# Performance work log

Measured on AMD Instinct MI355X. Metric: run time of the kernel, lower is better.

Reference implementation:

```python
import jax, jax.numpy as jnp
import numpy as np

N = 4096
IN_SIZE = 512
MLP_W = 16
HID = 512
MID = 64  # hardcoded tgc2 output size in the torch module
OUT = 128
BN_EPS = 1e-5


def setup_inputs() -> dict:
    key = jax.random.key(0)
    ks = jax.random.split(key, 24)
    adj = (jax.random.uniform(ks[0], (N, N)) < 0.05).astype(jnp.float32)
    xdeg = jax.random.uniform(ks[1], (N, N), dtype=jnp.float32)
    ydeg = jax.random.uniform(ks[2], (N, N), dtype=jnp.float32)
    u = lambda k, sh, fan: jax.random.uniform(k, sh, jnp.float32, -1.0, 1.0) / np.sqrt(fan)
    return {
        "adj": adj, "xdeg": xdeg, "ydeg": ydeg,
        # edge MLP: 3 -> MLP_W -> 2
        "mlp_w1": u(ks[3], (3, MLP_W), 3), "mlp_b1": jnp.zeros((MLP_W,), jnp.float32),
        "mlp_w2": u(ks[4], (MLP_W, 2), MLP_W), "mlp_b2": jnp.zeros((2,), jnp.float32),
        # positional linear: Linear(N, in_size) applied to eye(N) -> pe = W^T + b
        "pe_w": u(ks[5], (N, IN_SIZE), N), "pe_b": jnp.zeros((IN_SIZE,), jnp.float32),
        # GCN weights
        "gc1_w": u(ks[6], (IN_SIZE, HID), HID),
        "lin2_w": u(ks[7], (HID, MID), HID), "lin2_b": jnp.zeros((MID,), jnp.float32),
        "gc3_w": u(ks[8], (MID, OUT), OUT),
        # BatchNorm (eval mode: running stats)
        "bn1_g": jnp.ones((HID,), jnp.float32), "bn1_b": jnp.zeros((HID,), jnp.float32),
        "bn1_m": jnp.zeros((HID,), jnp.float32), "bn1_v": jnp.ones((HID,), jnp.float32),
        "bn2_g": jnp.ones((OUT,), jnp.float32), "bn2_b": jnp.zeros((OUT,), jnp.float32),
        "bn2_m": jnp.zeros((OUT,), jnp.float32), "bn2_v": jnp.ones((OUT,), jnp.float32),
    }


def reference(adj, xdeg, ydeg, mlp_w1, mlp_b1, mlp_w2, mlp_b2, pe_w, pe_b,
              gc1_w, lin2_w, lin2_b, gc3_w,
              bn1_g, bn1_b, bn1_m, bn1_v, bn2_g, bn2_b, bn2_m, bn2_v):
    # Edge MLP + softmax over [adj, xdeg, ydeg] features; torch only computes it
    # at nonzero adj entries then scatters into a dense mask. Since the mask is
    # multiplied by adj, computing densely and multiplying is exactly equivalent.
    feats = jnp.stack([adj, xdeg, ydeg], axis=-1)          # [N, N, 3]
    h = jax.nn.relu(jnp.einsum('nmf,fw->nmw', feats, mlp_w1) + mlp_b1)
    logits = jnp.einsum('nmw,wc->nmc', h, mlp_w2) + mlp_b2  # [N, N, 2]
    mask = jax.nn.softmax(logits, axis=-1)[..., 1]          # [N, N]
    a = adj * mask + jnp.eye(adj.shape[0], dtype=adj.dtype)

    # Degree normalization: A' = D_row^{-1/2} A D_col^{-1/2} (broadcast, no diag matmuls)
    rowsum = jnp.sum(a, axis=1)
    colsum = jnp.sum(a, axis=0)
    d_row = jnp.where(rowsum > 0, rowsum ** -0.5, 0.0)
    d_col = jnp.where(colsum > 0, colsum ** -0.5, 0.0)
    a = d_row[:, None] * a * d_col[None, :]

    # pe = Linear(eye(N)) = W^T + b (eval mode, dropout off)
    pe = pe_w + pe_b[None, :]                               # [N, IN_SIZE]

    h = a @ (pe @ gc1_w)                                    # GCN layer 1
    h = (h - bn1_m) * (bn1_g / jnp.sqrt(bn1_v + BN_EPS)) + bn1_b
    h = h @ lin2_w + lin2_b                                 # tgc2
    mid = h
    h = jax.nn.relu(h)
    h = a @ (h @ gc3_w)                                     # GCN layer 3
    out = (h - bn2_m) * (bn2_g / jnp.sqrt(bn2_v + BN_EPS)) + bn2_b
    return out, mid
```

## Files before the change

kernel.cpp:

```cpp
#include <hip/hip_runtime.h>
#include <hip/hip_bf16.h>

#define NN 4096
#define INS 512
#define HIDW 512
#define MIDW 64
#define OUTW 128
#define CAP 384
#define SEG 96
#define BN_EPS 1e-5f
#define CS_BLOCKS 256
#define CS_ROWS (NN / CS_BLOCKS)
#define NSTRIP 8
#define NPAIR (NSTRIP / 2)
#define SLOTCAP (NSTRIP * SEG)

__global__ __launch_bounds__(256) void k_count(
    const float* __restrict__ adj,
    int* __restrict__ cslot, int* __restrict__ cnt, int* __restrict__ dflag)
{
    const int t = threadIdx.x;
    const int wave = t >> 6, lane = t & 63;
    const int gw = blockIdx.x * 4 + wave;
    const int i = gw >> 3, s = gw & 7;
    const int colbase = s * 512;
    const float* __restrict__ base = adj + (size_t)i * NN + colbase + 4 * lane;
    float4 a4a = *reinterpret_cast<const float4*>(base);
    float4 a4b = *reinterpret_cast<const float4*>(base + 256);
    const float av[8] = {a4a.x, a4a.y, a4a.z, a4a.w,
                         a4b.x, a4b.y, a4b.z, a4b.w};
    int* __restrict__ slot = cslot + (size_t)i * SLOTCAP + s * SEG;
    const unsigned long long lt = (1ULL << lane) - 1ULL;
    int run = 0;
    #pragma unroll
    for (int c = 0; c < 8; ++c) {
        int col = colbase + ((c < 4) ? (4 * lane + c) : (256 + 4 * lane + c - 4));
        bool diag = (col == i);
        bool act = (av[c] != 0.f) || diag;
        if (diag) dflag[i] = (av[c] != 0.f) ? 1 : 0;
        unsigned long long m = __ballot(act);
        if (act) {
            int pos = run + __popcll(m & lt);
            if (pos < SEG) slot[pos] = col;
        }
        run += __popcll(m);
    }
    if (lane == 0) cnt[gw] = (run < SEG) ? run : SEG;
}

__global__ __launch_bounds__(256) void k_fill(
    const float* __restrict__ xdeg, const float* __restrict__ ydeg,
    const int* __restrict__ cslot, const int* __restrict__ cnt,
    const int* __restrict__ dflag,
    const float* __restrict__ w1, const float* __restrict__ b1,
    const float* __restrict__ w2, const float* __restrict__ b2,
    float* __restrict__ a_vals, int* __restrict__ a_cols,
    float* __restrict__ rs_part)
{
    __shared__ float shb[16], sw1x[16], sw1y[16], sw2[32], sb2[2];
    const int t = threadIdx.x;
    const int wave = t >> 6, lane = t & 63;
    if (t < 16) {
        shb[t]  = b1[t] + w1[t];
        sw1x[t] = w1[16 + t];
        sw1y[t] = w1[32 + t];
    }
    if (t < 32) sw2[t] = w2[t];
    if (t < 2)  sb2[t] = b2[t];
    __syncthreads();

    const int q = __builtin_amdgcn_readfirstlane(blockIdx.x * 4 + wave);
    const int i = q >> 2;
    const int sp = (q & 3) * 2;
    const int* __restrict__ cb = cnt + i * NSTRIP;
    int wb = 0;
    #pragma unroll
    for (int ss = 0; ss < NSTRIP; ++ss) if (ss < sp) wb += cb[ss];
    const int n0 = cb[sp];
    const int n1 = cb[sp + 1];
    const int ntot = n0 + n1;
    const int hasde = dflag[i];
    const int* __restrict__ slot = cslot + (size_t)i * SLOTCAP + sp * SEG;
    const float* __restrict__ xrow = xdeg + (size_t)i * NN;
    const float* __restrict__ yrow = ydeg + (size_t)i * NN;
    float* __restrict__ gv = a_vals + (size_t)i * CAP;
    int*   __restrict__ gc = a_cols + (size_t)i * CAP;

    float local = 0.f;
    for (int p = lane; p < ntot; p += 64) {
        int col = (p < n0) ? slot[p] : slot[SEG + p - n0];
        float x = xrow[col];
        float y = yrow[col];
        float l0 = sb2[0], l1 = sb2[1];
        #pragma unroll
        for (int w = 0; w < 16; ++w) {
            float hw = fmaf(x, sw1x[w], shb[w]);
            hw = fmaf(y, sw1y[w], hw);
            hw = fmaxf(hw, 0.f);
            l0 = fmaf(hw, sw2[2 * w],     l0);
            l1 = fmaf(hw, sw2[2 * w + 1], l1);
        }
        float v = 1.f / (1.f + __expf(l0 - l1));
        if (col == i) v = hasde ? (v + 1.f) : 1.f;
        int gp = wb + p;
        if (gp < CAP) { gc[gp] = col; gv[gp] = v; }
        local += v;
    }
    #pragma unroll
    for (int o = 32; o >= 1; o >>= 1)
        local += __shfl_down(local, o, 64);
    if (lane == 0) rs_part[q] = local;
}

__global__ __launch_bounds__(256) void k_colsum(
    const float* __restrict__ a_vals, const int* __restrict__ a_cols,
    const int* __restrict__ cnt, float* __restrict__ P)
{
    __shared__ float ls[NN];
    const int t = threadIdx.x;
    const int b = blockIdx.x;
    for (int j = t; j < NN; j += 256) ls[j] = 0.f;
    __syncthreads();
    const int r0 = b * CS_ROWS;
    for (int r = r0; r < r0 + CS_ROWS; ++r) {
        int n = 0;
        #pragma unroll
        for (int ss = 0; ss < NSTRIP; ++ss) n += cnt[r * NSTRIP + ss];
        n = (n < CAP) ? n : CAP;
        const float* __restrict__ vr = a_vals + (size_t)r * CAP;
        const int*   __restrict__ cr = a_cols + (size_t)r * CAP;
        for (int p = t; p < n; p += 256)
            atomicAdd(&ls[cr[p]], vr[p]);
    }
    __syncthreads();
    for (int j = t; j < NN; j += 256)
        P[(size_t)b * NN + j] = ls[j];
}

__global__ __launch_bounds__(512) void k_misc(
    const float* __restrict__ lin2_w, const float* __restrict__ lin2_b,
    const float* __restrict__ bn1_g, const float* __restrict__ bn1_b,
    const float* __restrict__ bn1_m, const float* __restrict__ bn1_v,
    const float* __restrict__ bn2_g, const float* __restrict__ bn2_b,
    const float* __restrict__ bn2_m, const float* __restrict__ bn2_v,
    const float* __restrict__ rs_part, const float* __restrict__ P,
    float* __restrict__ Wp, float* __restrict__ c1,
    float* __restrict__ s2g, float* __restrict__ t2g,
    float* __restrict__ d_row, float* __restrict__ d_col)
{
    const int t = threadIdx.x;
    if (blockIdx.x == 0) {
        __shared__ float t1s[HIDW];
        {
            int h = t;
            float s1 = bn1_g[h] * rsqrtf(bn1_v[h] + BN_EPS);
            t1s[h] = bn1_b[h] - bn1_m[h] * s1;
            for (int m = 0; m < MIDW; ++m)
                Wp[(size_t)h * MIDW + m] = s1 * lin2_w[(size_t)h * MIDW + m];
        }
        __syncthreads();
        if (t < MIDW) {
            float acc = lin2_b[t];
            for (int h = 0; h < HIDW; ++h)
                acc = fmaf(t1s[h], lin2_w[(size_t)h * MIDW + t], acc);
            c1[t] = acc;
        } else if (t >= 64 && t < 64 + OUTW) {
            int j = t - 64;
            float s2 = bn2_g[j] * rsqrtf(bn2_v[j] + BN_EPS);
            s2g[j] = s2;
            t2g[j] = bn2_b[j] - bn2_m[j] * s2;
        }
    } else {
        int j = (blockIdx.x - 1) * 512 + t;
        float r = 0.f;
        #pragma unroll
        for (int s = 0; s < NPAIR; ++s) r += rs_part[j * NPAIR + s];
        d_row[j] = (r > 0.f) ? 1.f / sqrtf(r) : 0.f;
        float c = 0.f;
        for (int b = 0; b < CS_BLOCKS; ++b)
            c += P[(size_t)b * NN + j];
        d_col[j] = (c > 0.f) ? 1.f / sqrtf(c) : 0.f;
    }
}

template <bool ABIAS, bool ROWSCALE>
__global__ __launch_bounds__(256) void k_thin(
    const float* __restrict__ A, const float* __restrict__ B,
    const float* __restrict__ abias, const float* __restrict__ rscale,
    float* __restrict__ C, int M, int K)
{
    __shared__ float As[64][36];
    __shared__ float Bs[64][64];
    const int t = threadIdx.x;
    const int bm = blockIdx.x * 32;
    const int c2 = t & 31, rg = t >> 5;

    float acc[4][2] = {};

    for (int k0 = 0; k0 < K; k0 += 64) {
        #pragma unroll
        for (int l = 0; l < 8; ++l) {
            int e = t + l * 256;
            int r = e >> 6, k = e & 63;
            float v = A[(size_t)(bm + r) * K + k0 + k];
            if (ABIAS) v += abias[k0 + k];
            As[k][r] = v;
        }
        #pragma unroll
        for (int l = 0; l < 16; ++l) {
            int e = t + l * 256;
            int k = e >> 6, n = e & 63;
            Bs[k][n] = B[(size_t)(k0 + k) * 64 + n];
        }
        __syncthreads();
        #pragma unroll
        for (int k = 0; k < 64; ++k) {
            float4 a4 = *reinterpret_cast<const float4*>(&As[k][rg * 4]);
            float2 b2 = *reinterpret_cast<const float2*>(&Bs[k][2 * c2]);
            acc[0][0] = fmaf(a4.x, b2.x, acc[0][0]);
            acc[0][1] = fmaf(a4.x, b2.y, acc[0][1]);
            acc[1][0] = fmaf(a4.y, b2.x, acc[1][0]);
            acc[1][1] = fmaf(a4.y, b2.y, acc[1][1]);
            acc[2][0] = fmaf(a4.z, b2.x, acc[2][0]);
            acc[2][1] = fmaf(a4.z, b2.y, acc[2][1]);
            acc[3][0] = fmaf(a4.w, b2.x, acc[3][0]);
            acc[3][1] = fmaf(a4.w, b2.y, acc[3][1]);
        }
        __syncthreads();
    }

    #pragma unroll
    for (int u = 0; u < 4; ++u) {
        int r = bm + rg * 4 + u;
        float sc = ROWSCALE ? rscale[r] : 1.f;
        float2 o = make_float2(acc[u][0] * sc, acc[u][1] * sc);
        *reinterpret_cast<float2*>(&C[(size_t)r * 64 + 2 * c2]) = o;
    }
}

template <bool WITH_MID>
__global__ __launch_bounds__(256) void k_spmm(
    const float* __restrict__ a_vals, const int* __restrict__ a_cols,
    const int* __restrict__ cnt, const float* __restrict__ X,
    const float* __restrict__ d_row, const float* __restrict__ d_col,
    const float* __restrict__ c1,
    const float* __restrict__ gc3, const float* __restrict__ s2g,
    const float* __restrict__ t2g,
    float* __restrict__ O1, float* __restrict__ O2)
{
    __shared__ float sv[2][CAP];
    __shared__ int   scl[2][CAP];
    __shared__ float sacc[4][64];
    const int t = threadIdx.x;
    const int wave = t >> 6, lane = t & 63;
    const int rb = wave >> 1, h = wave & 1;
    const int i = blockIdx.x * 2 + rb;
    int n = 0;
    #pragma unroll
    for (int ss = 0; ss < NSTRIP; ++ss) n += cnt[i * NSTRIP + ss];
    n = (n < CAP) ? n : CAP;
    const int n16 = (n + 15) & ~15;
    const float* __restrict__ vrow = a_vals + (size_t)i * CAP;
    const int*   __restrict__ crow = a_cols + (size_t)i * CAP;

    for (int p = h * 64 + lane; p < n16; p += 128) {
        bool ok = p < n;
        sv[rb][p]  = ok ? vrow[p] : 0.f;
        scl[rb][p] = ok ? crow[p] : 0;
    }
    __syncthreads();

    const int eh = lane >> 5;
    const int lc = lane & 31;
    const int Q  = n16 >> 1;
    const int Qh = Q >> 1;

    float a0 = 0.f, a1 = 0.f;
    for (int q = h * Qh; q < (h + 1) * Qh; q += 4) {
        #pragma unroll
        for (int j = 0; j < 4; ++j) {
            int p = 2 * (q + j) + eh;
            float v = sv[rb][p];
            int c = scl[rb][p];
            float2 x = *reinterpret_cast<const float2*>(X + (size_t)c * 64 + 2 * lc);
            a0 = fmaf(v, x.x, a0);
            a1 = fmaf(v, x.y, a1);
        }
    }
    a0 += __shfl_xor(a0, 32);
    a1 += __shfl_xor(a1, 32);
    if (lane < 32) { sacc[wave][2 * lc] = a0; sacc[wave][2 * lc + 1] = a1; }
    __syncthreads();

    if (WITH_MID) {
        if (h == 0 && lane < 32) {
            float s0 = sacc[wave][2 * lc]     + sacc[wave + 1][2 * lc];
            float s1 = sacc[wave][2 * lc + 1] + sacc[wave + 1][2 * lc + 1];
            float dr = d_row[i];
            float dc = d_col[i];
            float m0 = fmaf(s0, dr, c1[2 * lc]);
            float m1 = fmaf(s1, dr, c1[2 * lc + 1]);
            *reinterpret_cast<float2*>(O1 + (size_t)i * 64 + 2 * lc) =
                make_float2(m0, m1);
            *reinterpret_cast<float2*>(O2 + (size_t)i * 64 + 2 * lc) =
                make_float2(dc * fmaxf(m0, 0.f), dc * fmaxf(m1, 0.f));
        }
    } else {
        if (h == 0 && lane < 32) {
            float dr = d_row[i];
            float s0 = (sacc[wave][2 * lc]     + sacc[wave + 1][2 * lc])     * dr;
            float s1 = (sacc[wave][2 * lc + 1] + sacc[wave + 1][2 * lc + 1]) * dr;
            sacc[wave][2 * lc]     = s0;
            sacc[wave][2 * lc + 1] = s1;
        }
        __syncthreads();
        const int rb2 = t >> 7;
        const int j = t & 127;
        const float* __restrict__ srow = sacc[2 * rb2];
        float acc = 0.f;
        #pragma unroll 8
        for (int k = 0; k < 64; ++k)
            acc = fmaf(srow[k], gc3[k * 128 + j], acc);
        int orow = blockIdx.x * 2 + rb2;
        O1[(size_t)orow * 128 + j] = fmaf(acc, s2g[j], t2g[j]);
    }
}

extern "C" void kernel_launch(void* const* d_in, const int* in_sizes, int n_in,
                              void* d_out, int out_size, void* d_ws, size_t ws_size,
                              hipStream_t stream) {
    const float* adj    = (const float*)d_in[0];
    const float* xdeg   = (const float*)d_in[1];
    const float* ydeg   = (const float*)d_in[2];
    const float* mlp_w1 = (const float*)d_in[3];
    const float* mlp_b1 = (const float*)d_in[4];
    const float* mlp_w2 = (const float*)d_in[5];
    const float* mlp_b2 = (const float*)d_in[6];
    const float* pe_w   = (const float*)d_in[7];
    const float* pe_b   = (const float*)d_in[8];
    const float* gc1_w  = (const float*)d_in[9];
    const float* lin2_w = (const float*)d_in[10];
    const float* lin2_b = (const float*)d_in[11];
    const float* gc3_w  = (const float*)d_in[12];
    const float* bn1_g  = (const float*)d_in[13];
    const float* bn1_b  = (const float*)d_in[14];
    const float* bn1_m  = (const float*)d_in[15];
    const float* bn1_v  = (const float*)d_in[16];
    const float* bn2_g  = (const float*)d_in[17];
    const float* bn2_b  = (const float*)d_in[18];
    const float* bn2_m  = (const float*)d_in[19];
    const float* bn2_v  = (const float*)d_in[20];

    float* out = (float*)d_out;
    float* mid = out + (size_t)NN * OUTW;

    char* w = (char*)d_ws;
    float* a_vals = (float*)w;  w += (size_t)NN * CAP * 4;
    int*   a_cols = (int*)w;    w += (size_t)NN * CAP * 4;
    int*   cslot  = (int*)w;    w += (size_t)NN * SLOTCAP * 4;
    int*   cnt    = (int*)w;    w += (size_t)NN * NSTRIP * 4;
    int*   dflag  = (int*)w;    w += (size_t)NN * 4;
    float* rs_part= (float*)w;  w += (size_t)NN * NPAIR * 4;
    float* d_row  = (float*)w;  w += (size_t)NN * 4;
    float* d_col  = (float*)w;  w += (size_t)NN * 4;
    float* P      = (float*)w;  w += (size_t)CS_BLOCKS * NN * 4;
    float* Wp     = (float*)w;  w += (size_t)HIDW * MIDW * 4;
    float* W2     = (float*)w;  w += (size_t)INS * MIDW * 4;
    float* c1     = (float*)w;  w += 256;
    float* s2g    = (float*)w;  w += 512;
    float* t2g    = (float*)w;  w += 512;
    float* G      = (float*)w;  w += (size_t)NN * MIDW * 4;
    float* R      = (float*)w;  w += (size_t)NN * MIDW * 4;

    k_count<<<NN * NSTRIP / 4, 256, 0, stream>>>(adj, cslot, cnt, dflag);
    k_fill<<<NN * NPAIR / 4, 256, 0, stream>>>(
        xdeg, ydeg, cslot, cnt, dflag, mlp_w1, mlp_b1, mlp_w2, mlp_b2,
        a_vals, a_cols, rs_part);
    k_colsum<<<CS_BLOCKS, 256, 0, stream>>>(a_vals, a_cols, cnt, P);
    k_misc<<<9, 512, 0, stream>>>(lin2_w, lin2_b, bn1_g, bn1_b, bn1_m, bn1_v,
                                  bn2_g, bn2_b, bn2_m, bn2_v, rs_part, P,
                                  Wp, c1, s2g, t2g, d_row, d_col);
    k_thin<false, false><<<INS / 32, 256, 0, stream>>>(
        gc1_w, Wp, nullptr, nullptr, W2, INS, HIDW);
    k_thin<true, true><<<NN / 32, 256, 0, stream>>>(
        pe_w, W2, pe_b, d_col, G, NN, INS);
    k_spmm<true><<<NN / 2, 256, 0, stream>>>(
        a_vals, a_cols, cnt, G, d_row, d_col, c1,
        nullptr, nullptr, nullptr, mid, R);
    k_spmm<false><<<NN / 2, 256, 0, stream>>>(
        a_vals, a_cols, cnt, R, d_row, d_col, nullptr,
        gc3_w, s2g, t2g, out, nullptr);
}
```

Baseline: 133.1 us.

## Merge independent dense GEMMs into sparse-prep kernels to cut launches

The kernel sequence is regrouped so independent work shares a launch. The BN/lin2 weight prep runs as an extra block of the count kernel, the gc1_w×Wp product runs as extra blocks of the fill kernel, and the pe×W2 product runs alongside the column-sum kernel. To allow this, the d_col row scaling moves out of the G GEMM and into the first SpMM's value staging, so G no longer waits on d_col. This removes two kernel launches and their serial dependencies. The cost is one extra d_col gather per nonzero in the SpMM, and heterogeneous blocks inside one grid that may balance unevenly.

```diff
diff --git a/kernel.cpp b/kernel.cpp
--- a/kernel.cpp
+++ b/kernel.cpp
@@ -15,144 +15,71 @@
 #define NPAIR (NSTRIP / 2)
 #define SLOTCAP (NSTRIP * SEG)
 
-__global__ __launch_bounds__(256) void k_count(
+__device__ __forceinline__ void thin_block(
+    const float* __restrict__ A, const float* __restrict__ B,
+    const float* __restrict__ abias, float* __restrict__ C, int K, int bb)
+{
+    __shared__ float As[64][36];
+    __shared__ float Bs[64][64];
+    const int t = threadIdx.x;
+    const int bm = bb * 32;
+    const int c2 = t & 31, rg = t >> 5;
+
+    float acc[4][2] = {};
+    for (int k0 = 0; k0 < K; k0 += 64) {
+        #pragma unroll
+        for (int l = 0; l < 8; ++l) {
+            int e = t + l * 256;
+            int r = e >> 6, k = e & 63;
+            float v = A[(size_t)(bm + r) * K + k0 + k];
+            if (abias) v += abias[k0 + k];
+            As[k][r] = v;
+        }
+        #pragma unroll
+        for (int l = 0; l < 16; ++l) {
+            int e = t + l * 256;
+            int k = e >> 6, n = e & 63;
+            Bs[k][n] = B[(size_t)(k0 + k) * 64 + n];
+        }
+        __syncthreads();
+        #pragma unroll
+        for (int k = 0; k < 64; ++k) {
+            float4 a4 = *reinterpret_cast<const float4*>(&As[k][rg * 4]);
+            float2 b2 = *reinterpret_cast<const float2*>(&Bs[k][2 * c2]);
+            acc[0][0] = fmaf(a4.x, b2.x, acc[0][0]);
+            acc[0][1] = fmaf(a4.x, b2.y, acc[0][1]);
+            acc[1][0] = fmaf(a4.y, b2.x, acc[1][0]);
+            acc[1][1] = fmaf(a4.y, b2.y, acc[1][1]);
+            acc[2][0] = fmaf(a4.z, b2.x, acc[2][0]);
+            acc[2][1] = fmaf(a4.z, b2.y, acc[2][1]);
+            acc[3][0] = fmaf(a4.w, b2.x, acc[3][0]);
+            acc[3][1] = fmaf(a4.w, b2.y, acc[3][1]);
+        }
+        __syncthreads();
+    }
+    #pragma unroll
+    for (int u = 0; u < 4; ++u) {
+        int r = bm + rg * 4 + u;
+        *reinterpret_cast<float2*>(&C[(size_t)r * 64 + 2 * c2]) =
+            make_float2(acc[u][0], acc[u][1]);
+    }
+}
+
+__global__ __launch_bounds__(256) void k_count_prep(
     const float* __restrict__ adj,
-    int* __restrict__ cslot, int* __restrict__ cnt, int* __restrict__ dflag)
-{
-    const int t = threadIdx.x;
-    const int wave = t >> 6, lane = t & 63;
-    const int gw = blockIdx.x * 4 + wave;
-    const int i = gw >> 3, s = gw & 7;
-    const int colbase = s * 512;
-    const float* __restrict__ base = adj + (size_t)i * NN + colbase + 4 * lane;
-    float4 a4a = *reinterpret_cast<const float4*>(base);
-    float4 a4b = *reinterpret_cast<const float4*>(base + 256);
-    const float av[8] = {a4a.x, a4a.y, a4a.z, a4a.w,
-                         a4b.x, a4b.y, a4b.z, a4b.w};
-    int* __restrict__ slot = cslot + (size_t)i * SLOTCAP + s * SEG;
-    const unsigned long long lt = (1ULL << lane) - 1ULL;
-    int run = 0;
-    #pragma unroll
-    for (int c = 0; c < 8; ++c) {
-        int col = colbase + ((c < 4) ? (4 * lane + c) : (256 + 4 * lane + c - 4));
-        bool diag = (col == i);
-        bool act = (av[c] != 0.f) || diag;
-        if (diag) dflag[i] = (av[c] != 0.f) ? 1 : 0;
-        unsigned long long m = __ballot(act);
-        if (act) {
-            int pos = run + __popcll(m & lt);
-            if (pos < SEG) slot[pos] = col;
-        }
-        run += __popcll(m);
-    }
-    if (lane == 0) cnt[gw] = (run < SEG) ? run : SEG;
-}
-
-__global__ __launch_bounds__(256) void k_fill(
-    const float* __restrict__ xdeg, const float* __restrict__ ydeg,
-    const int* __restrict__ cslot, const int* __restrict__ cnt,
-    const int* __restrict__ dflag,
-    const float* __restrict__ w1, const float* __restrict__ b1,
-    const float* __restrict__ w2, const float* __restrict__ b2,
-    float* __restrict__ a_vals, int* __restrict__ a_cols,
-    float* __restrict__ rs_part)
-{
-    __shared__ float shb[16], sw1x[16], sw1y[16], sw2[32], sb2[2];
-    const int t = threadIdx.x;
-    const int wave = t >> 6, lane = t & 63;
-    if (t < 16) {
-        shb[t]  = b1[t] + w1[t];
-        sw1x[t] = w1[16 + t];
-        sw1y[t] = w1[32 + t];
-    }
-    if (t < 32) sw2[t] = w2[t];
-    if (t < 2)  sb2[t] = b2[t];
-    __syncthreads();
-
-    const int q = __builtin_amdgcn_readfirstlane(blockIdx.x * 4 + wave);
-    const int i = q >> 2;
-    const int sp = (q & 3) * 2;
-    const int* __restrict__ cb = cnt + i * NSTRIP;
-    int wb = 0;
-    #pragma unroll
-    for (int ss = 0; ss < NSTRIP; ++ss) if (ss < sp) wb += cb[ss];
-    const int n0 = cb[sp];
-    const int n1 = cb[sp + 1];
-    const int ntot = n0 + n1;
-    const int hasde = dflag[i];
-    const int* __restrict__ slot = cslot + (size_t)i * SLOTCAP + sp * SEG;
-    const float* __restrict__ xrow = xdeg + (size_t)i * NN;
-    const float* __restrict__ yrow = ydeg + (size_t)i * NN;
-    float* __restrict__ gv = a_vals + (size_t)i * CAP;
-    int*   __restrict__ gc = a_cols + (size_t)i * CAP;
-
-    float local = 0.f;
-    for (int p = lane; p < ntot; p += 64) {
-        int col = (p < n0) ? slot[p] : slot[SEG + p - n0];
-        float x = xrow[col];
-        float y = yrow[col];
-        float l0 = sb2[0], l1 = sb2[1];
-        #pragma unroll
-        for (int w = 0; w < 16; ++w) {
-            float hw = fmaf(x, sw1x[w], shb[w]);
-            hw = fmaf(y, sw1y[w], hw);
-            hw = fmaxf(hw, 0.f);
-            l0 = fmaf(hw, sw2[2 * w],     l0);
-            l1 = fmaf(hw, sw2[2 * w + 1], l1);
-        }
-        float v = 1.f / (1.f + __expf(l0 - l1));
-        if (col == i) v = hasde ? (v + 1.f) : 1.f;
-        int gp = wb + p;
-        if (gp < CAP) { gc[gp] = col; gv[gp] = v; }
-        local += v;
-    }
-    #pragma unroll
-    for (int o = 32; o >= 1; o >>= 1)
-        local += __shfl_down(local, o, 64);
-    if (lane == 0) rs_part[q] = local;
-}
-
-__global__ __launch_bounds__(256) void k_colsum(
-    const float* __restrict__ a_vals, const int* __restrict__ a_cols,
-    const int* __restrict__ cnt, float* __restrict__ P)
-{
-    __shared__ float ls[NN];
-    const int t = threadIdx.x;
-    const int b = blockIdx.x;
-    for (int j = t; j < NN; j += 256) ls[j] = 0.f;
-    __syncthreads();
-    const int r0 = b * CS_ROWS;
-    for (int r = r0; r < r0 + CS_ROWS; ++r) {
-        int n = 0;
-        #pragma unroll
-        for (int ss = 0; ss < NSTRIP; ++ss) n += cnt[r * NSTRIP + ss];
-        n = (n < CAP) ? n : CAP;
-        const float* __restrict__ vr = a_vals + (size_t)r * CAP;
-        const int*   __restrict__ cr = a_cols + (size_t)r * CAP;
-        for (int p = t; p < n; p += 256)
-            atomicAdd(&ls[cr[p]], vr[p]);
-    }
-    __syncthreads();
-    for (int j = t; j < NN; j += 256)
-        P[(size_t)b * NN + j] = ls[j];
-}
-
-__global__ __launch_bounds__(512) void k_misc(
+    int* __restrict__ cslot, int* __restrict__ cnt, int* __restrict__ dflag,
     const float* __restrict__ lin2_w, const float* __restrict__ lin2_b,
     const float* __restrict__ bn1_g, const float* __restrict__ bn1_b,
     const float* __restrict__ bn1_m, const float* __restrict__ bn1_v,
     const float* __restrict__ bn2_g, const float* __restrict__ bn2_b,
     const float* __restrict__ bn2_m, const float* __restrict__ bn2_v,
-    const float* __restrict__ rs_part, const float* __restrict__ P,
     float* __restrict__ Wp, float* __restrict__ c1,
-    float* __restrict__ s2g, float* __restrict__ t2g,
-    float* __restrict__ d_row, float* __restrict__ d_col)
+    float* __restrict__ s2g, float* __restrict__ t2g)
 {
     const int t = threadIdx.x;
     if (blockIdx.x == 0) {
         __shared__ float t1s[HIDW];
-        {
-            int h = t;
+        for (int h = t; h < HIDW; h += 256) {
             float s1 = bn1_g[h] * rsqrtf(bn1_v[h] + BN_EPS);
             t1s[h] = bn1_b[h] - bn1_m[h] * s1;
             for (int m = 0; m < MIDW; ++m)
@@ -170,72 +97,150 @@
             s2g[j] = s2;
             t2g[j] = bn2_b[j] - bn2_m[j] * s2;
         }
-    } else {
-        int j = (blockIdx.x - 1) * 512 + t;
-        float r = 0.f;
-        #pragma unroll
-        for (int s = 0; s < NPAIR; ++s) r += rs_part[j * NPAIR + s];
-        d_row[j] = (r > 0.f) ? 1.f / sqrtf(r) : 0.f;
-        float c = 0.f;
-        for (int b = 0; b < CS_BLOCKS; ++b)
-            c += P[(size_t)b * NN + j];
-        d_col[j] = (c > 0.f) ? 1.f / sqrtf(c) : 0.f;
-    }
-}
-
-template <bool ABIAS, bool ROWSCALE>
-__global__ __launch_bounds__(256) void k_thin(
-    const float* __restrict__ A, const float* __restrict__ B,
-    const float* __restrict__ abias, const float* __restrict__ rscale,
-    float* __restrict__ C, int M, int K)
-{
-    __shared__ float As[64][36];
-    __shared__ float Bs[64][64];
-    const int t = threadIdx.x;
-    const int bm = blockIdx.x * 32;
-    const int c2 = t & 31, rg = t >> 5;
-
-    float acc[4][2] = {};
-
-    for (int k0 = 0; k0 < K; k0 += 64) {
-        #pragma unroll
-        for (int l = 0; l < 8; ++l) {
-            int e = t + l * 256;
-            int r = e >> 6, k = e & 63;
-            float v = A[(size_t)(bm + r) * K + k0 + k];
-            if (ABIAS) v += abias[k0 + k];
-            As[k][r] = v;
-        }
-        #pragma unroll
-        for (int l = 0; l < 16; ++l) {
-            int e = t + l * 256;
-            int k = e >> 6, n = e & 63;
-            Bs[k][n] = B[(size_t)(k0 + k) * 64 + n];
-        }
-        __syncthreads();
-        #pragma unroll
-        for (int k = 0; k < 64; ++k) {
-            float4 a4 = *reinterpret_cast<const float4*>(&As[k][rg * 4]);
-            float2 b2 = *reinterpret_cast<const float2*>(&Bs[k][2 * c2]);
-            acc[0][0] = fmaf(a4.x, b2.x, acc[0][0]);
-            acc[0][1] = fmaf(a4.x, b2.y, acc[0][1]);
-            acc[1][0] = fmaf(a4.y, b2.x, acc[1][0]);
-            acc[1][1] = fmaf(a4.y, b2.y, acc[1][1]);
-            acc[2][0] = fmaf(a4.z, b2.x, acc[2][0]);
-            acc[2][1] = fmaf(a4.z, b2.y, acc[2][1]);
-            acc[3][0] = fmaf(a4.w, b2.x, acc[3][0]);
-            acc[3][1] = fmaf(a4.w, b2.y, acc[3][1]);
-        }
-        __syncthreads();
-    }
-
-    #pragma unroll
-    for (int u = 0; u < 4; ++u) {
-        int r = bm + rg * 4 + u;
-        float sc = ROWSCALE ? rscale[r] : 1.f;
-        float2 o = make_float2(acc[u][0] * sc, acc[u][1] * sc);
-        *reinterpret_cast<float2*>(&C[(size_t)r * 64 + 2 * c2]) = o;
-    }
+        return;
+    }
+    const int wave = t >> 6, lane = t & 63;
+    const int gw = (blockIdx.x - 1) * 4 + wave;
+    const int i = gw >> 3, s = gw & 7;
+    const int colbase = s * 512;
+    const float* __restrict__ base = adj + (size_t)i * NN + colbase + 4 * lane;
+    float4 a4a = *reinterpret_cast<const float4*>(base);
+    float4 a4b = *reinterpret_cast<const float4*>(base + 256);
+    const float av[8] = {a4a.x, a4a.y, a4a.z, a4a.w,
+                         a4b.x, a4b.y, a4b.z, a4b.w};
+    int* __restrict__ slot = cslot + (size_t)i * SLOTCAP + s * SEG;
+    const unsigned long long lt = (1ULL << lane) - 1ULL;
+    int run = 0;
+    #pragma unroll
+    for (int c = 0; c < 8; ++c) {
+        int col = colbase + ((c < 4) ? (4 * lane + c) : (256 + 4 * lane + c - 4));
+        bool diag = (col == i);
+        bool act = (av[c] != 0.f) || diag;
+        if (diag) dflag[i] = (av[c] != 0.f) ? 1 : 0;
+        unsigned long long m = __ballot(act);
+        if (act) {
+            int pos = run + __popcll(m & lt);
+            if (pos < SEG) slot[pos] = col;
+        }
+        run += __popcll(m);
+    }
+    if (lane == 0) cnt[gw] = (run < SEG) ? run : SEG;
+}
+
+__global__ __launch_bounds__(256) void k_fill_w2(
+    const float* __restrict__ xdeg, const float* __restrict__ ydeg,
+    const int* __restrict__ cslot, const int* __restrict__ cnt,
+    const int* __restrict__ dflag,
+    const float* __restrict__ w1, const float* __restrict__ b1,
+    const float* __restrict__ w2, const float* __restrict__ b2,
+    float* __restrict__ a_vals, int* __restrict__ a_cols,
+    float* __restrict__ rs_part,
+    const float* __restrict__ gc1_w, const float* __restrict__ Wp,
+    float* __restrict__ W2)
+{
+    if (blockIdx.x < INS / 32) {
+        thin_block(gc1_w, Wp, nullptr, W2, HIDW, blockIdx.x);
+        return;
+    }
+    __shared__ float shb[16], sw1x[16], sw1y[16], sw2[32], sb2[2];
+    const int t = threadIdx.x;
+    const int wave = t >> 6, lane = t & 63;
+    if (t < 16) {
+        shb[t]  = b1[t] + w1[t];
+        sw1x[t] = w1[16 + t];
+        sw1y[t] = w1[32 + t];
+    }
+    if (t < 32) sw2[t] = w2[t];
+    if (t < 2)  sb2[t] = b2[t];
+    __syncthreads();
+
+    const int q = __builtin_amdgcn_readfirstlane(
+        (blockIdx.x - INS / 32) * 4 + wave);
+    const int i = q >> 2;
+    const int sp = (q & 3) * 2;
+    const int* __restrict__ cb = cnt + i * NSTRIP;
+    int wb = 0;
+    #pragma unroll
+    for (int ss = 0; ss < NSTRIP; ++ss) if (ss < sp) wb += cb[ss];
+    const int n0 = cb[sp];
+    const int ntot = n0 + cb[sp + 1];
+    const int hasde = dflag[i];
+    const int* __restrict__ slot = cslot + (size_t)i * SLOTCAP + sp * SEG;
+    const float* __restrict__ xrow = xdeg + (size_t)i * NN;
+    const float* __restrict__ yrow = ydeg + (size_t)i * NN;
+    float* __restrict__ gv = a_vals + (size_t)i * CAP;
+    int*   __restrict__ gc = a_cols + (size_t)i * CAP;
+
+    float local = 0.f;
+    for (int p = lane; p < ntot; p += 64) {
+        int col = (p < n0) ? slot[p] : slot[SEG + p - n0];
+        float x = xrow[col];
+        float y = yrow[col];
+        float l0 = sb2[0], l1 = sb2[1];
+        #pragma unroll
+        for (int w = 0; w < 16; ++w) {
+            float hw = fmaf(x, sw1x[w], shb[w]);
+            hw = fmaf(y, sw1y[w], hw);
+            hw = fmaxf(hw, 0.f);
+            l0 = fmaf(hw, sw2[2 * w],     l0);
+            l1 = fmaf(hw, sw2[2 * w + 1], l1);
+        }
+        float v = 1.f / (1.f + __expf(l0 - l1));
+        if (col == i) v = hasde ? (v + 1.f) : 1.f;
+        int gp = wb + p;
+        if (gp < CAP) { gc[gp] = col; gv[gp] = v; }
+        local += v;
+    }
+    #pragma unroll
+    for (int o = 32; o >= 1; o >>= 1)
+        local += __shfl_down(local, o, 64);
+    if (lane == 0) rs_part[q] = local;
+}
+
+__global__ __launch_bounds__(256) void k_colsum_g(
+    const float* __restrict__ a_vals, const int* __restrict__ a_cols,
+    const int* __restrict__ cnt, float* __restrict__ P,
+    const float* __restrict__ pe_w, const float* __restrict__ pe_b,
+    const float* __restrict__ W2, float* __restrict__ G)
+{
+    if (blockIdx.x < NN / 32) {
+        thin_block(pe_w, W2, pe_b, G, INS, blockIdx.x);
+        return;
+    }
+    __shared__ float ls[NN];
+    const int t = threadIdx.x;
+    const int b = blockIdx.x - NN / 32;
+    for (int j = t; j < NN; j += 256) ls[j] = 0.f;
+    __syncthreads();
+    const int r0 = b * CS_ROWS;
+    for (int r = r0; r < r0 + CS_ROWS; ++r) {
+        int n = 0;
+        #pragma unroll
+        for (int ss = 0; ss < NSTRIP; ++ss) n += cnt[r * NSTRIP + ss];
+        n = (n < CAP) ? n : CAP;
+        const float* __restrict__ vr = a_vals + (size_t)r * CAP;
+        const int*   __restrict__ cr = a_cols + (size_t)r * CAP;
+        for (int p = t; p < n; p += 256)
+            atomicAdd(&ls[cr[p]], vr[p]);
+    }
+    __syncthreads();
+    for (int j = t; j < NN; j += 256)
+        P[(size_t)b * NN + j] = ls[j];
+}
+
+__global__ __launch_bounds__(512) void k_scale(
+    const float* __restrict__ rs_part, const float* __restrict__ P,
+    float* __restrict__ d_row, float* __restrict__ d_col)
+{
+    int j = blockIdx.x * 512 + threadIdx.x;
+    float r = 0.f;
+    #pragma unroll
+    for (int s = 0; s < NPAIR; ++s) r += rs_part[j * NPAIR + s];
+    d_row[j] = (r > 0.f) ? 1.f / sqrtf(r) : 0.f;
+    float c = 0.f;
+    for (int b = 0; b < CS_BLOCKS; ++b)
+        c += P[(size_t)b * NN + j];
+    d_col[j] = (c > 0.f) ? 1.f / sqrtf(c) : 0.f;
 }
 
 template <bool WITH_MID>
@@ -265,8 +270,11 @@
 
     for (int p = h * 64 + lane; p < n16; p += 128) {
         bool ok = p < n;
-        sv[rb][p]  = ok ? vrow[p] : 0.f;
-        scl[rb][p] = ok ? crow[p] : 0;
+        int c = ok ? crow[p] : 0;
+        float v = ok ? vrow[p] : 0.f;
+        if (WITH_MID) v *= d_col[c];
+        sv[rb][p]  = v;
+        scl[rb][p] = c;
     }
     __syncthreads();
 
@@ -372,18 +380,15 @@
     float* G      = (float*)w;  w += (size_t)NN * MIDW * 4;
     float* R      = (float*)w;  w += (size_t)NN * MIDW * 4;
 
-    k_count<<<NN * NSTRIP / 4, 256, 0, stream>>>(adj, cslot, cnt, dflag);
-    k_fill<<<NN * NPAIR / 4, 256, 0, stream>>>(
+    k_count_prep<<<NN * NSTRIP / 4 + 1, 256, 0, stream>>>(
+        adj, cslot, cnt, dflag, lin2_w, lin2_b, bn1_g, bn1_b, bn1_m, bn1_v,
+        bn2_g, bn2_b, bn2_m, bn2_v, Wp, c1, s2g, t2g);
+    k_fill_w2<<<INS / 32 + NN * NPAIR / 4, 256, 0, stream>>>(
         xdeg, ydeg, cslot, cnt, dflag, mlp_w1, mlp_b1, mlp_w2, mlp_b2,
-        a_vals, a_cols, rs_part);
-    k_colsum<<<CS_BLOCKS, 256, 0, stream>>>(a_vals, a_cols, cnt, P);
-    k_misc<<<9, 512, 0, stream>>>(lin2_w, lin2_b, bn1_g, bn1_b, bn1_m, bn1_v,
-                                  bn2_g, bn2_b, bn2_m, bn2_v, rs_part, P,
-                                  Wp, c1, s2g, t2g, d_row, d_col);
-    k_thin<false, false><<<INS / 32, 256, 0, stream>>>(
-        gc1_w, Wp, nullptr, nullptr, W2, INS, HIDW);
-    k_thin<true, true><<<NN / 32, 256, 0, stream>>>(
-        pe_w, W2, pe_b, d_col, G, NN, INS);
+        a_vals, a_cols, rs_part, gc1_w, Wp, W2);
+    k_colsum_g<<<NN / 32 + CS_BLOCKS, 256, 0, stream>>>(
+        a_vals, a_cols, cnt, P, pe_w, pe_b, W2, G);
+    k_scale<<<NN / 512, 512, 0, stream>>>(rs_part, P, d_row, d_col);
     k_spmm<true><<<NN / 2, 256, 0, stream>>>(
         a_vals, a_cols, cnt, G, d_row, d_col, c1,
         nullptr, nullptr, nullptr, mid, R);
```

New measurement: 129.7 us. 1.03x faster.
